# Optimization experiments

Hardware: AMD Instinct MI355X
Metric: run time of the kernel (lower is better)

The kernel has to match this reference:

```python
import jax, jax.numpy as jnp
import numpy as np

B, D, NT, NZ = 16384, 64, 128, 2048


def setup_inputs() -> dict:
    key = jax.random.key(0)
    ks = jax.random.split(key, 5)
    return {
        "t": jax.random.uniform(ks[0], (1,), dtype=jnp.float32),
        "z": jax.random.normal(ks[1], (B, D), dtype=jnp.float32),
        "logp_z": jnp.zeros((B, 1), jnp.float32),
        "centres_z": jax.random.normal(ks[2], (NZ, D), dtype=jnp.float32),
        "log_sigmas_z": jnp.zeros((NZ,), jnp.float32),
        "centres_t": jax.random.normal(ks[3], (NT, 1), dtype=jnp.float32),
        "log_sigmas_t": jnp.zeros((NT,), jnp.float32),
        "W": 0.01 * jax.random.normal(ks[4], (D, NT, NZ + 1), dtype=jnp.float32),
    }


def _gauss(r):
    return jnp.exp(-r * r)


def _forward(t, z, centres_z, log_sigmas_z, centres_t, log_sigmas_t, W):
    # time RBF features Phi_t: (NT,)
    r_t = jnp.abs(t.reshape(1, 1) - centres_t.reshape(1, -1)) / jnp.exp(log_sigmas_t)
    phi_t = _gauss(r_t).reshape(-1)
    W_t = jnp.einsum('dij,i->dj', W, phi_t)  # (D, NZ+1)
    Wz, bias = W_t[:, :-1], W_t[:, -1]       # bias comes from the appended ones column
    # z RBF features via squared-distance identity (avoids [B,NZ,D] blowup)
    sq = (jnp.sum(z * z, axis=1, keepdims=True)
          + jnp.sum(centres_z * centres_z, axis=1)[None, :]
          - 2.0 * z @ centres_z.T)
    sq = jnp.maximum(sq, 0.0)                 # (B, NZ) squared distances
    inv_s2 = jnp.exp(-2.0 * log_sigmas_z)     # 1/sigma_j^2, (NZ,)
    phi_z = jnp.exp(-sq * inv_s2)             # gaussian(||z-c_j||/s_j), (B, NZ)
    dz_dt = phi_z @ Wz.T + bias               # (B, D)
    # exact Jacobian trace for gaussian basis:
    #   d phi_j / d z_i = -2 * phi_j * (z_i - c_{j,i}) / s_j^2
    #   tr(J)_b = sum_j phi_{b,j} * inv_s2_j * (-2) * (sum_i Wz[i,j] z_{b,i} - sum_i Wz[i,j] c_{j,i})
    q = jnp.einsum('dj,jd->j', Wz, centres_z)  # (NZ,)
    trace = -2.0 * jnp.sum(phi_z * inv_s2 * (z @ Wz - q), axis=1)  # (B,)
    dlogp_z_dt = -trace[:, None]               # (B, 1)
    return dz_dt, dlogp_z_dt


def reference(t, z, logp_z, centres_z, log_sigmas_z, centres_t, log_sigmas_t, W):
    return _forward(t, z, centres_z, log_sigmas_z, centres_t, log_sigmas_t, W)
```

## Files before the change

kernel.cpp:

```cpp
#include <hip/hip_runtime.h>
#include <math.h>

typedef unsigned int uint;
typedef unsigned short ushort;
typedef unsigned char uchar;
typedef __attribute__((ext_vector_type(4))) float f32x4;

#define BB  16384
#define DD  64
#define NT_ 128
#define NZ_ 2048
#define NJ_ 2049

#define BIAS_OFF 0
#define SCS_OFF  64
#define ZF8A_OFF 8256
#define ZF8B_OFF 139328
#define ZZG_OFF  270400
#define CZ8A_OFF 286784
#define CZ8B_OFF 303168
#define WZ8A_OFF 319552
#define WZ8B_OFF 335936
#define WZBP_OFF 352320
#define PART_OFF 417856

#if __has_builtin(__builtin_amdgcn_cvt_pk_fp8_f32)
__device__ __forceinline__ uint pk4_fp8(float a, float b, float c, float d) {
  int v = __builtin_amdgcn_cvt_pk_fp8_f32(a, b, 0, false);
  v = __builtin_amdgcn_cvt_pk_fp8_f32(c, d, v, true);
  return (uint)v;
}
__device__ __forceinline__ uchar f8_1(float x) {
  return (uchar)(__builtin_amdgcn_cvt_pk_fp8_f32(x, x, 0, false) & 0xFF);
}
#else
__device__ __forceinline__ uint sw_f8(float x) {
  uint u = __float_as_uint(x);
  uint s = (u >> 24) & 0x80u;
  float ax = __uint_as_float(u & 0x7FFFFFFFu);
  if (!(ax >= 0.015625f)) return s;
  if (ax >= 448.f) return s | 0x7Eu;
  uint q = __float_as_uint(ax);
  q += 0x7FFFFu + ((q >> 20) & 1u);
  uint e = (q >> 23) - 120u;
  return s | ((e & 0xFu) << 3) | ((q >> 20) & 7u);
}
__device__ __forceinline__ uchar f8_1(float x) { return (uchar)sw_f8(x); }
__device__ __forceinline__ uint pk4_fp8(float a, float b, float c, float d) {
  return sw_f8(a) | (sw_f8(b) << 8) | (sw_f8(c) << 16) | (sw_f8(d) << 24);
}
#endif

__global__ __launch_bounds__(256) void k_wt1(
    const float* __restrict__ t, const float* __restrict__ ct,
    const float* __restrict__ lst, const float* __restrict__ W,
    float* __restrict__ part)
{
  __shared__ float ph[32];
  int tx = threadIdx.x;
  int d  = blockIdx.y;
  int ic = blockIdx.z;
  if (tx < 32) {
    int i = ic * 32 + tx;
    float r = fabsf(t[0] - ct[i]) * __expf(-lst[i]);
    ph[tx] = __expf(-r * r);
  }
  __syncthreads();
  int j = blockIdx.x * 256 + tx;
  if (j >= NJ_) return;
  const float* Wp = W + (size_t)d * NT_ * NJ_ + (size_t)(ic * 32) * NJ_ + j;
  float acc = 0.f;
#pragma unroll
  for (int k = 0; k < 32; ++k) acc += Wp[(size_t)k * NJ_] * ph[k];
  part[((size_t)ic * 64 + d) * NJ_ + j] = acc;
}

__global__ __launch_bounds__(256) void k_prep2(
    const float* __restrict__ part, const float* __restrict__ cz,
    const float* __restrict__ lsz,
    float* __restrict__ bias, float4* __restrict__ scs,
    uchar* __restrict__ cz8a, uchar* __restrict__ cz8b,
    uchar* __restrict__ wz8a, uchar* __restrict__ wz8b,
    uchar* __restrict__ wzbp8)
{
  __shared__ float wt[64][9];
  int tid = threadIdx.x;
  int cb0 = blockIdx.x * 8;
#pragma unroll
  for (int h = 0; h < 2; ++h) {
    int f = h * 256 + tid;
    int d = f >> 3, c = f & 7;
    size_t idx = (size_t)d * NJ_ + cb0 + c;
    float s = part[idx] + part[(size_t)64 * NJ_ + idx]
            + part[(size_t)128 * NJ_ + idx] + part[(size_t)192 * NJ_ + idx];
    wt[d][c] = s;
    int cg = cb0 + c;
    wzbp8[((size_t)(cg >> 5) * 64 + d) * 32 + (cg & 31)] = f8_1(s);
  }
  if (blockIdx.x == 0 && tid < 64) {
    size_t idx = (size_t)tid * NJ_ + 2048;
    bias[tid] = part[idx] + part[(size_t)64 * NJ_ + idx]
              + part[(size_t)128 * NJ_ + idx] + part[(size_t)192 * NJ_ + idx];
  }
  __syncthreads();
  int cl = tid >> 5;
  int k  = tid & 31;
  int c  = cb0 + cl;
  float cv0 = cz[(size_t)c * DD + k];
  float cv1 = cz[(size_t)c * DD + 32 + k];
  cz8a[(size_t)c * 32 + k] = f8_1(cv0);
  cz8b[(size_t)c * 32 + k] = f8_1(cv1);
  float w0 = wt[k][cl], w1 = wt[32 + k][cl];
  wz8a[(size_t)c * 32 + k] = f8_1(w0);
  wz8b[(size_t)c * 32 + k] = f8_1(w1);
  float ca = cv0 * cv0 + cv1 * cv1;
  float qa = w0 * cv0 + w1 * cv1;
  qa += __shfl_xor(qa, 1);  ca += __shfl_xor(ca, 1);
  qa += __shfl_xor(qa, 2);  ca += __shfl_xor(ca, 2);
  qa += __shfl_xor(qa, 4);  ca += __shfl_xor(ca, 4);
  qa += __shfl_xor(qa, 8);  ca += __shfl_xor(ca, 8);
  qa += __shfl_xor(qa, 16); ca += __shfl_xor(ca, 16);
  if (k == 0) scs[c] = make_float4(ca, __expf(-2.f * lsz[c]), qa, 0.f);
}

__global__ __launch_bounds__(256) void k_zbp(
    const float* __restrict__ z, uchar* __restrict__ zf8a,
    uchar* __restrict__ zf8b, float* __restrict__ zzg)
{
  int g = blockIdx.x * 256 + threadIdx.x;
  int r = g >> 3, s8 = g & 7;
  const float4* zp = (const float4*)(z + (size_t)r * DD + s8 * 8);
  float4 v0 = zp[0], v1 = zp[1];
  uint lo = pk4_fp8(v0.x, v0.y, v0.z, v0.w);
  uint hi = pk4_fp8(v1.x, v1.y, v1.z, v1.w);
  uchar* dst = (s8 < 4 ? zf8a : zf8b) + (size_t)r * 32 + (s8 & 3) * 8;
  *(uint2*)dst = make_uint2(lo, hi);
  float ss = v0.x * v0.x + v0.y * v0.y + v0.z * v0.z + v0.w * v0.w
           + v1.x * v1.x + v1.y * v1.y + v1.z * v1.z + v1.w * v1.w;
  ss += __shfl_xor(ss, 1);
  ss += __shfl_xor(ss, 2);
  ss += __shfl_xor(ss, 4);
  if (s8 == 0) zzg[r] = ss;
}

#define PH_LD 40

__global__ __launch_bounds__(256) void k_fused(
    const uchar* __restrict__ zf8a, const uchar* __restrict__ zf8b,
    const float* __restrict__ zzg,
    const uchar* __restrict__ cz8a, const uchar* __restrict__ cz8b,
    const uchar* __restrict__ wz8a, const uchar* __restrict__ wz8b,
    const uchar* __restrict__ wzbp8,
    const float4* __restrict__ scs, const float* __restrict__ bias,
    float* __restrict__ out)
{
  __shared__ char smem[10240];
  __shared__ float dlr[4][32];
  uchar* phs = (uchar*)smem;
  float* eps = (float*)smem;

  int tid  = threadIdx.x;
  int ws   = tid >> 6;
  int lane = tid & 63;
  int lrow = lane & 15, quad = lane >> 4;
  int b0 = blockIdx.x * 32;

  long az[2][2];
#pragma unroll
  for (int mt = 0; mt < 2; ++mt) {
    size_t ro = (size_t)(b0 + mt * 16 + lrow) * 32 + quad * 8;
    az[mt][0] = *(const long*)(zf8a + ro);
    az[mt][1] = *(const long*)(zf8b + ro);
  }
  float zzr[2][4];
#pragma unroll
  for (int mt = 0; mt < 2; ++mt) {
    float v = zzg[b0 + mt * 16 + lrow];
#pragma unroll
    for (int i = 0; i < 4; ++i) zzr[mt][i] = __shfl(v, quad * 4 + i);
  }

  f32x4 acc[2][4];
#pragma unroll
  for (int mt = 0; mt < 2; ++mt)
#pragma unroll
    for (int nt = 0; nt < 4; ++nt) acc[mt][nt] = (f32x4){0.f, 0.f, 0.f, 0.f};
  float dl[2][4] = {{0.f}};

  const f32x4 zero = (f32x4){0.f, 0.f, 0.f, 0.f};
  int cbase = ws * 512;
  int pbase = ws * 32 * PH_LD;

  long Abc0[2][2], Abc1[2][2], Abw0[2][2], Abw1[2][2], Abb[2][4];
  float4 Asc[2][2];
#define LOADB(PAR, C0)                                                         \
  do {                                                                         \
    int c0_ = (C0);                                                            \
    _Pragma("unroll")                                                          \
    for (int nt = 0; nt < 2; ++nt) {                                           \
      int cg_ = c0_ + nt * 16 + lrow;                                          \
      size_t ro_ = (size_t)cg_ * 32 + quad * 8;                                \
      Abc0[PAR][nt] = *(const long*)(cz8a + ro_);                              \
      Abc1[PAR][nt] = *(const long*)(cz8b + ro_);                              \
      Abw0[PAR][nt] = *(const long*)(wz8a + ro_);                              \
      Abw1[PAR][nt] = *(const long*)(wz8b + ro_);                              \
      Asc[PAR][nt]  = scs[cg_];                                                \
    }                                                                          \
    size_t cb_ = (size_t)(c0_ >> 5) * 64 * 32;                                 \
    _Pragma("unroll")                                                          \
    for (int nt = 0; nt < 4; ++nt)                                             \
      Abb[PAR][nt] =                                                           \
          *(const long*)(wzbp8 + cb_ + (size_t)(nt * 16 + lrow) * 32 + quad * 8); \
  } while (0)

  LOADB(0, cbase);
#pragma unroll 2
  for (int it = 0; it < 16; ++it) {
    int par = it & 1;
    LOADB(par ^ 1, cbase + ((it + 1) & 15) * 32);

    int pb = par * (4 * 32 * PH_LD) + pbase;
#pragma unroll
    for (int nt = 0; nt < 2; ++nt) {
      float4 sc = Asc[par][nt];
#pragma unroll
      for (int mt = 0; mt < 2; ++mt) {
        f32x4 d1 = __builtin_amdgcn_mfma_f32_16x16x32_fp8_fp8(az[mt][0], Abc0[par][nt], zero, 0, 0, 0);
        d1       = __builtin_amdgcn_mfma_f32_16x16x32_fp8_fp8(az[mt][1], Abc1[par][nt], d1,   0, 0, 0);
        f32x4 d2 = __builtin_amdgcn_mfma_f32_16x16x32_fp8_fp8(az[mt][0], Abw0[par][nt], zero, 0, 0, 0);
        d2       = __builtin_amdgcn_mfma_f32_16x16x32_fp8_fp8(az[mt][1], Abw1[par][nt], d2,   0, 0, 0);
#pragma unroll
        for (int i = 0; i < 4; ++i) {
          float s = zzr[mt][i] + sc.x - 2.f * d1[i];
          s = fmaxf(s, 0.f);
          float p = __expf(-s * sc.y);
          dl[mt][i] += p * sc.y * (d2[i] - sc.z);
          phs[pb + (mt * 16 + quad * 4 + i) * PH_LD + nt * 16 + lrow] = f8_1(p);
        }
      }
    }
    long ap0 = *(const long*)&phs[pb + lrow * PH_LD + quad * 8];
    long ap1 = *(const long*)&phs[pb + (16 + lrow) * PH_LD + quad * 8];
#pragma unroll
    for (int nt = 0; nt < 4; ++nt) {
      acc[0][nt] = __builtin_amdgcn_mfma_f32_16x16x32_fp8_fp8(ap0, Abb[par][nt], acc[0][nt], 0, 0, 0);
      acc[1][nt] = __builtin_amdgcn_mfma_f32_16x16x32_fp8_fp8(ap1, Abb[par][nt], acc[1][nt], 0, 0, 0);
    }
  }
#undef LOADB

#pragma unroll
  for (int mt = 0; mt < 2; ++mt)
#pragma unroll
    for (int i = 0; i < 4; ++i) {
      float v = dl[mt][i];
      v += __shfl_xor(v, 1);
      v += __shfl_xor(v, 2);
      v += __shfl_xor(v, 4);
      v += __shfl_xor(v, 8);
      if (lrow == 0) dlr[ws][mt * 16 + quad * 4 + i] = v;
    }

  for (int s = 0; s < 4; ++s) {
    __syncthreads();
    if (ws == s) {
#pragma unroll
      for (int mt = 0; mt < 2; ++mt)
#pragma unroll
        for (int nt = 0; nt < 4; ++nt)
#pragma unroll
          for (int i = 0; i < 4; ++i) {
            int r = mt * 16 + quad * 4 + i;
            int d = nt * 16 + lrow;
            if (s == 0) eps[r * 68 + d] = acc[mt][nt][i];
            else        eps[r * 68 + d] += acc[mt][nt][i];
          }
    }
  }
  __syncthreads();

  {
    int r = tid >> 3, d0 = (tid & 7) * 8;
    float4 e0 = *(const float4*)&eps[r * 68 + d0];
    float4 e1 = *(const float4*)&eps[r * 68 + d0 + 4];
    float4 bv0 = *(const float4*)&bias[d0];
    float4 bv1 = *(const float4*)&bias[d0 + 4];
    float4 o0, o1;
    o0.x = e0.x + bv0.x; o0.y = e0.y + bv0.y; o0.z = e0.z + bv0.z; o0.w = e0.w + bv0.w;
    o1.x = e1.x + bv1.x; o1.y = e1.y + bv1.y; o1.z = e1.z + bv1.z; o1.w = e1.w + bv1.w;
    *(float4*)&out[(size_t)(b0 + r) * DD + d0]     = o0;
    *(float4*)&out[(size_t)(b0 + r) * DD + d0 + 4] = o1;
  }
  if (tid < 32) {
    float s = dlr[0][tid] + dlr[1][tid] + dlr[2][tid] + dlr[3][tid];
    out[(size_t)BB * DD + b0 + tid] = 2.f * s;
  }
}

extern "C" void kernel_launch(void* const* d_in, const int* in_sizes, int n_in,
                              void* d_out, int out_size, void* d_ws, size_t ws_size,
                              hipStream_t stream)
{
  const float* t   = (const float*)d_in[0];
  const float* z   = (const float*)d_in[1];
  const float* cz  = (const float*)d_in[3];
  const float* lsz = (const float*)d_in[4];
  const float* ct  = (const float*)d_in[5];
  const float* lst = (const float*)d_in[6];
  const float* W   = (const float*)d_in[7];
  float* out = (float*)d_out;
  float* ws  = (float*)d_ws;

  float*  bias = ws + BIAS_OFF;
  float4* scs  = (float4*)(ws + SCS_OFF);
  uchar*  zf8a = (uchar*)(ws + ZF8A_OFF);
  uchar*  zf8b = (uchar*)(ws + ZF8B_OFF);
  float*  zzg  = ws + ZZG_OFF;
  uchar*  cz8a = (uchar*)(ws + CZ8A_OFF);
  uchar*  cz8b = (uchar*)(ws + CZ8B_OFF);
  uchar*  wz8a = (uchar*)(ws + WZ8A_OFF);
  uchar*  wz8b = (uchar*)(ws + WZ8B_OFF);
  uchar*  wzbp8 = (uchar*)(ws + WZBP_OFF);
  float*  part = ws + PART_OFF;

  k_wt1<<<dim3(9, 64, 4), 256, 0, stream>>>(t, ct, lst, W, part);
  k_prep2<<<dim3(256), 256, 0, stream>>>(part, cz, lsz, bias, scs,
                                         cz8a, cz8b, wz8a, wz8b, wzbp8);
  k_zbp<<<dim3(512), 256, 0, stream>>>(z, zf8a, zf8b, zzg);
  k_fused<<<dim3(BB / 32), 256, 0, stream>>>(zf8a, zf8b, zzg, cz8a, cz8b,
                                             wz8a, wz8b, wzbp8, scs, bias, out);
}
```

Measured before the change: 141.6 us.

## Fuse z fp8 conversion into main kernel, use raw exp2, prioritize MFMA

Removes the separate k_zbp kernel: the fused kernel now loads z in fp32, packs it to fp8 in registers and computes the row squared norm with cross-lane shuffles. This drops one launch and the round trip of the fp8 z buffer through global memory. The Gaussian exponent is folded into a single FMA scaled by a precomputed inv*log2(e) and evaluated with the native v_exp_f32 instruction. The B-matrix MFMA block is wrapped in s_setprio so matrix work gets issue priority. The trade-off is that every block now reads fp32 z directly, four times the bytes of the fp8 copy.

```diff
diff --git a/kernel.cpp b/kernel.cpp
--- a/kernel.cpp
+++ b/kernel.cpp
@@ -4,6 +4,7 @@
 typedef unsigned int uint;
 typedef unsigned short ushort;
 typedef unsigned char uchar;
+typedef unsigned long ulong_;
 typedef __attribute__((ext_vector_type(4))) float f32x4;
 
 #define BB  16384
@@ -14,15 +15,12 @@
 
 #define BIAS_OFF 0
 #define SCS_OFF  64
-#define ZF8A_OFF 8256
-#define ZF8B_OFF 139328
-#define ZZG_OFF  270400
-#define CZ8A_OFF 286784
-#define CZ8B_OFF 303168
-#define WZ8A_OFF 319552
-#define WZ8B_OFF 335936
-#define WZBP_OFF 352320
-#define PART_OFF 417856
+#define CZ8A_OFF 8256
+#define CZ8B_OFF 24640
+#define WZ8A_OFF 41024
+#define WZ8B_OFF 57408
+#define WZBP_OFF 73792
+#define PART_OFF 106560
 
 #if __has_builtin(__builtin_amdgcn_cvt_pk_fp8_f32)
 __device__ __forceinline__ uint pk4_fp8(float a, float b, float c, float d) {
@@ -120,34 +118,16 @@
   qa += __shfl_xor(qa, 4);  ca += __shfl_xor(ca, 4);
   qa += __shfl_xor(qa, 8);  ca += __shfl_xor(ca, 8);
   qa += __shfl_xor(qa, 16); ca += __shfl_xor(ca, 16);
-  if (k == 0) scs[c] = make_float4(ca, __expf(-2.f * lsz[c]), qa, 0.f);
-}
-
-__global__ __launch_bounds__(256) void k_zbp(
-    const float* __restrict__ z, uchar* __restrict__ zf8a,
-    uchar* __restrict__ zf8b, float* __restrict__ zzg)
-{
-  int g = blockIdx.x * 256 + threadIdx.x;
-  int r = g >> 3, s8 = g & 7;
-  const float4* zp = (const float4*)(z + (size_t)r * DD + s8 * 8);
-  float4 v0 = zp[0], v1 = zp[1];
-  uint lo = pk4_fp8(v0.x, v0.y, v0.z, v0.w);
-  uint hi = pk4_fp8(v1.x, v1.y, v1.z, v1.w);
-  uchar* dst = (s8 < 4 ? zf8a : zf8b) + (size_t)r * 32 + (s8 & 3) * 8;
-  *(uint2*)dst = make_uint2(lo, hi);
-  float ss = v0.x * v0.x + v0.y * v0.y + v0.z * v0.z + v0.w * v0.w
-           + v1.x * v1.x + v1.y * v1.y + v1.z * v1.z + v1.w * v1.w;
-  ss += __shfl_xor(ss, 1);
-  ss += __shfl_xor(ss, 2);
-  ss += __shfl_xor(ss, 4);
-  if (s8 == 0) zzg[r] = ss;
+  if (k == 0) {
+    float inv = __expf(-2.f * lsz[c]);
+    scs[c] = make_float4(ca, inv, qa, inv * 1.44269504f);
+  }
 }
 
 #define PH_LD 40
 
 __global__ __launch_bounds__(256) void k_fused(
-    const uchar* __restrict__ zf8a, const uchar* __restrict__ zf8b,
-    const float* __restrict__ zzg,
+    const float* __restrict__ z,
     const uchar* __restrict__ cz8a, const uchar* __restrict__ cz8b,
     const uchar* __restrict__ wz8a, const uchar* __restrict__ wz8b,
     const uchar* __restrict__ wzbp8,
@@ -166,18 +146,28 @@
   int b0 = blockIdx.x * 32;
 
   long az[2][2];
+  float zzr[2][4];
 #pragma unroll
   for (int mt = 0; mt < 2; ++mt) {
-    size_t ro = (size_t)(b0 + mt * 16 + lrow) * 32 + quad * 8;
-    az[mt][0] = *(const long*)(zf8a + ro);
-    az[mt][1] = *(const long*)(zf8b + ro);
-  }
-  float zzr[2][4];
-#pragma unroll
-  for (int mt = 0; mt < 2; ++mt) {
-    float v = zzg[b0 + mt * 16 + lrow];
-#pragma unroll
-    for (int i = 0; i < 4; ++i) zzr[mt][i] = __shfl(v, quad * 4 + i);
+    const float* zr = z + (size_t)(b0 + mt * 16 + lrow) * DD + quad * 8;
+    float4 v0 = *(const float4*)zr;
+    float4 v1 = *(const float4*)(zr + 4);
+    float4 v2 = *(const float4*)(zr + 32);
+    float4 v3 = *(const float4*)(zr + 36);
+    uint l0 = pk4_fp8(v0.x, v0.y, v0.z, v0.w);
+    uint l1 = pk4_fp8(v1.x, v1.y, v1.z, v1.w);
+    uint h0 = pk4_fp8(v2.x, v2.y, v2.z, v2.w);
+    uint h1 = pk4_fp8(v3.x, v3.y, v3.z, v3.w);
+    az[mt][0] = (long)(((ulong_)l1 << 32) | l0);
+    az[mt][1] = (long)(((ulong_)h1 << 32) | h0);
+    float ss = v0.x * v0.x + v0.y * v0.y + v0.z * v0.z + v0.w * v0.w
+             + v1.x * v1.x + v1.y * v1.y + v1.z * v1.z + v1.w * v1.w
+             + v2.x * v2.x + v2.y * v2.y + v2.z * v2.z + v2.w * v2.w
+             + v3.x * v3.x + v3.y * v3.y + v3.z * v3.z + v3.w * v3.w;
+    ss += __shfl_xor(ss, 16);
+    ss += __shfl_xor(ss, 32);
+#pragma unroll
+    for (int i = 0; i < 4; ++i) zzr[mt][i] = __shfl(ss, quad * 4 + i);
   }
 
   f32x4 acc[2][4];
@@ -231,9 +221,10 @@
         d2       = __builtin_amdgcn_mfma_f32_16x16x32_fp8_fp8(az[mt][1], Abw1[par][nt], d2,   0, 0, 0);
 #pragma unroll
         for (int i = 0; i < 4; ++i) {
-          float s = zzr[mt][i] + sc.x - 2.f * d1[i];
-          s = fmaxf(s, 0.f);
-          float p = __expf(-s * sc.y);
+          float e = fmaf(d1[i], 2.f, -(zzr[mt][i] + sc.x)) * sc.w;
+          e = fminf(e, 0.f);
+          float p;
+          asm("v_exp_f32 %0, %1" : "=v"(p) : "v"(e));
           dl[mt][i] += p * sc.y * (d2[i] - sc.z);
           phs[pb + (mt * 16 + quad * 4 + i) * PH_LD + nt * 16 + lrow] = f8_1(p);
         }
@@ -241,11 +232,13 @@
     }
     long ap0 = *(const long*)&phs[pb + lrow * PH_LD + quad * 8];
     long ap1 = *(const long*)&phs[pb + (16 + lrow) * PH_LD + quad * 8];
+    __builtin_amdgcn_s_setprio(1);
 #pragma unroll
     for (int nt = 0; nt < 4; ++nt) {
       acc[0][nt] = __builtin_amdgcn_mfma_f32_16x16x32_fp8_fp8(ap0, Abb[par][nt], acc[0][nt], 0, 0, 0);
       acc[1][nt] = __builtin_amdgcn_mfma_f32_16x16x32_fp8_fp8(ap1, Abb[par][nt], acc[1][nt], 0, 0, 0);
     }
+    __builtin_amdgcn_s_setprio(0);
   }
 #undef LOADB
 
@@ -313,9 +306,6 @@
 
   float*  bias = ws + BIAS_OFF;
   float4* scs  = (float4*)(ws + SCS_OFF);
-  uchar*  zf8a = (uchar*)(ws + ZF8A_OFF);
-  uchar*  zf8b = (uchar*)(ws + ZF8B_OFF);
-  float*  zzg  = ws + ZZG_OFF;
   uchar*  cz8a = (uchar*)(ws + CZ8A_OFF);
   uchar*  cz8b = (uchar*)(ws + CZ8B_OFF);
   uchar*  wz8a = (uchar*)(ws + WZ8A_OFF);
@@ -326,7 +316,6 @@
   k_wt1<<<dim3(9, 64, 4), 256, 0, stream>>>(t, ct, lst, W, part);
   k_prep2<<<dim3(256), 256, 0, stream>>>(part, cz, lsz, bias, scs,
                                          cz8a, cz8b, wz8a, wz8b, wzbp8);
-  k_zbp<<<dim3(512), 256, 0, stream>>>(z, zf8a, zf8b, zzg);
-  k_fused<<<dim3(BB / 32), 256, 0, stream>>>(zf8a, zf8b, zzg, cz8a, cz8b,
+  k_fused<<<dim3(BB / 32), 256, 0, stream>>>(z, cz8a, cz8b,
                                              wz8a, wz8b, wzbp8, scs, bias, out);
 }
```

Measured after the change: 138.7 us. -2.1%, faster.
